# Optimization experiments

Measured on AMD Instinct MI355X. Metric: run time of the kernel, lower is better.

The kernel has to match this reference:

```python
import jax, jax.numpy as jnp
import numpy as np

TEMPERATURE = 0.5


def setup_inputs() -> dict:
    key = jax.random.key(0)
    ks = jax.random.split(key, 12)
    B, N, T = 128, 64, 256
    IN, H, OUT = N + T, 256, 128
    E = N * (N - 1) // 2  # 2016 upper-tri edges per graph
    total_edges = B * E
    inp = {
        "x_topology": jax.random.normal(ks[0], (B, N, N), jnp.float32),
        "x_temporal": jax.random.normal(ks[1], (B, N, T), jnp.float32),
        "gumbel_u": jax.random.uniform(ks[2], (total_edges,), jnp.float32, 1e-6, 1.0),
        # GNNLayer linear
        "W_gnn": jax.random.normal(ks[3], (IN, H), jnp.float32) / np.sqrt(IN),
        "b_gnn": jnp.zeros((H,), jnp.float32),
        # edge heads (input dim 2*H)
        "W_mean": jax.random.normal(ks[4], (2 * H, OUT), jnp.float32) / np.sqrt(2 * H),
        "b_mean": jnp.zeros((OUT,), jnp.float32),
        "W_var": jax.random.normal(ks[5], (2 * H, OUT), jnp.float32) / np.sqrt(2 * H),
        "b_var": jnp.zeros((OUT,), jnp.float32),
        "W_w": jax.random.normal(ks[6], (2 * H, 1), jnp.float32) / np.sqrt(2 * H),
        "b_w": jnp.zeros((1,), jnp.float32),
    }
    return inp


def reference(x_topology, x_temporal, gumbel_u, W_gnn, b_gnn,
              W_mean, b_mean, W_var, b_var, W_w, b_w):
    B, N, _ = x_topology.shape
    T = x_temporal.shape[-1]
    # Upper-triangular fully-connected edge index (no self loops), batched with node offsets.
    row, col = jnp.triu_indices(N, k=1)          # [E]
    E = row.shape[0]
    offs = (jnp.arange(B) * N)[:, None]          # [B,1]
    src = (row[None, :] + offs).reshape(-1)       # [B*E]
    dst = (col[None, :] + offs).reshape(-1)       # [B*E]

    # Node features: concat topology + temporal, flatten batch of graphs.
    x = jnp.concatenate([x_topology, x_temporal], axis=-1).reshape(B * N, N + T)

    # Mean aggregation (PyG aggr='mean'): messages x[src] scattered to dst; 0 for isolated nodes.
    msg_sum = jax.ops.segment_sum(x[src], dst, num_segments=B * N)      # [B*N, N+T]
    cnt = jax.ops.segment_sum(jnp.ones_like(src, x.dtype), dst, num_segments=B * N)
    agg = jnp.where(cnt[:, None] > 0, msg_sum / jnp.maximum(cnt, 1.0)[:, None], 0.0)

    h = jax.nn.relu(agg @ W_gnn + b_gnn)          # [B*N, H]

    # Edge MLP heads on gathered [src||dst] embeddings.
    ef = jnp.concatenate([h[src], h[dst]], axis=-1)        # [B*E, 2H]
    mean = ef @ W_mean + b_mean                             # [B*E, OUT]
    variance = jax.nn.softplus(ef @ W_var + b_var) + 1e-6   # [B*E, OUT]
    weight = jax.nn.sigmoid((ef @ W_w + b_w)[:, 0])          # [B*E]

    # Gumbel-softmax over the flattened edge-weight vector (dim=-1 of a 1-D tensor).
    g = -jnp.log(-jnp.log(gumbel_u))
    gumbel_w = jax.nn.softmax((weight + g) / TEMPERATURE, axis=-1)

    # Gaussian similarity per edge, scatter into dense adjacency.
    sim = jnp.exp(-0.5 * jnp.mean(mean ** 2 / (variance + 1e-8), axis=-1))
    edge_w = sim * gumbel_w                                  # [B*E]

    b_idx = jnp.repeat(jnp.arange(B), E)
    adj = jnp.zeros((B, N, N), x.dtype).at[b_idx, jnp.tile(row, B), jnp.tile(col, B)].set(edge_w)
    return adj
```

## Files before the change

### kernel.cpp

```cpp
#include <hip/hip_runtime.h>
#include <hip/hip_bf16.h>
#include <math.h>

#define Bg   128
#define Nn   64
#define Tt   256
#define INF  320
#define Hd   256
#define OUTD 128
#define Ee   2016
#define TOTE (Bg*Ee)
#define SCOLS 576
#define MROWS 8192

typedef __attribute__((ext_vector_type(8))) short bf16x8;
typedef __attribute__((ext_vector_type(4))) float f32x4;

static __device__ __forceinline__ ushort f2bf(float v) {
    __hip_bfloat16 h = __float2bfloat16(v);
    return *(ushort*)&h;
}

#define CVT_N (INF * Hd)
#define PACK_N (Hd * SCOLS)
__global__ void k_prep(const float* __restrict__ Wg, const float* __restrict__ Wm,
                       const float* __restrict__ Wv, const float* __restrict__ Ww,
                       const float* __restrict__ bm, const float* __restrict__ bv,
                       const float* __restrict__ bw,
                       ushort* __restrict__ WgbT, ushort* __restrict__ WcatT,
                       float* __restrict__ ebias, unsigned* __restrict__ red) {
    int idx = blockIdx.x * 256 + threadIdx.x;
    if (idx == 0) { red[0] = 0u; red[1] = 0u; }
    if (idx < CVT_N) {
        int n = idx / INF, k = idx - n * INF;
        WgbT[idx] = f2bf(Wg[k * Hd + n]);
        return;
    }
    idx -= CVT_N;
    if (idx < PACK_N) {
        int n = idx / Hd, k = idx - n * Hd;
        float v = 0.f;
        if (n < 128)       v = Wm[k * 128 + n];
        else if (n < 256)  v = Wm[(256 + k) * 128 + (n - 128)];
        else if (n < 384)  v = Wv[k * 128 + (n - 256)];
        else if (n < 512)  v = Wv[(256 + k) * 128 + (n - 384)];
        else if (n == 512) v = Ww[k];
        else if (n == 513) v = Ww[256 + k];
        WcatT[idx] = f2bf(v);
        return;
    }
    idx -= PACK_N;
    if (idx >= SCOLS) return;
    float e = 0.f;
    if (idx < 128)                    e = bm[idx];
    else if (idx >= 256 && idx < 384) e = bv[idx - 256];
    else if (idx == 512)              e = bw[0];
    ebias[idx] = e;
}

__global__ __launch_bounds__(256) void k_agg(const float* __restrict__ topo,
                                             const float* __restrict__ temp,
                                             ushort* __restrict__ agg) {
    __shared__ float T[64 * 65];
    const int b = blockIdx.x, ft = blockIdx.y;
    const int tid = threadIdx.x;
    const int row = tid >> 2, seg = tid & 3;
    const float* src = (ft == 0) ? (topo + (size_t)(b * Nn + row) * Nn)
                                 : (temp + (size_t)(b * Nn + row) * Tt + (ft - 1) * 64);
    #pragma unroll
    for (int i = 0; i < 4; ++i) {
        float4 v = *(const float4*)(src + seg * 16 + i * 4);
        float* d = &T[row * 65 + seg * 16 + i * 4];
        d[0] = v.x; d[1] = v.y; d[2] = v.z; d[3] = v.w;
    }
    __syncthreads();
    const int w = tid >> 6, lane = tid & 63;
    #pragma unroll
    for (int k = 0; k < 16; ++k) {
        int f = w * 16 + k;
        float x = T[lane * 65 + f];
        float incl = x;
        #pragma unroll
        for (int o = 1; o < 64; o <<= 1) {
            float t = __shfl_up(incl, o);
            if (lane >= o) incl += t;
        }
        float excl = incl - x;
        T[lane * 65 + f] = lane ? excl * __builtin_amdgcn_rcpf((float)lane) : 0.f;
    }
    __syncthreads();
    const int node = tid >> 2, f0 = (tid & 3) * 16;
    ushort tmp[16];
    #pragma unroll
    for (int i = 0; i < 16; ++i) tmp[i] = f2bf(T[node * 65 + f0 + i]);
    ushort* dst = agg + (size_t)(b * Nn + node) * INF + ft * 64 + f0;
    *(uint4*)dst = *(uint4*)tmp;
    *(uint4*)(dst + 8) = *(uint4*)(tmp + 8);
}

__global__ __launch_bounds__(256) void k_gemm_mfma(const ushort* __restrict__ A,
                                                   const ushort* __restrict__ BT,
                                                   const float* __restrict__ bias,
                                                   ushort* __restrict__ Cb,
                                                   float* __restrict__ Cf,
                                                   int N, int K, int relu, int transC) {
    __shared__ ushort Asl[64 * 72];
    __shared__ ushort Bsl[64 * 72];
    const int tid = threadIdx.x;
    const int w = tid >> 6, lane = tid & 63;
    const int quad = lane >> 4, r16 = lane & 15;
    const int m0 = blockIdx.y * 64, n0 = blockIdx.x * 64;
    const int row = tid >> 2, seg = tid & 3;
    f32x4 acc[4] = {};

    for (int k0 = 0; k0 < K; k0 += 64) {
        const ushort* ap = A + (size_t)(m0 + row) * K + k0 + seg * 16;
        uint4 a0 = ((const uint4*)ap)[0];
        uint4 a1 = ((const uint4*)ap)[1];
        *(uint4*)(Asl + row * 72 + seg * 16)     = a0;
        *(uint4*)(Asl + row * 72 + seg * 16 + 8) = a1;
        const ushort* bp = BT + (size_t)(n0 + row) * K + k0 + seg * 16;
        uint4 b0 = ((const uint4*)bp)[0];
        uint4 b1 = ((const uint4*)bp)[1];
        *(uint4*)(Bsl + row * 72 + seg * 16)     = b0;
        *(uint4*)(Bsl + row * 72 + seg * 16 + 8) = b1;
        __syncthreads();

        bf16x8 af0 = *(const bf16x8*)(Asl + (w * 16 + r16) * 72 + quad * 8);
        bf16x8 af1 = *(const bf16x8*)(Asl + (w * 16 + r16) * 72 + 32 + quad * 8);
        #pragma unroll
        for (int ns = 0; ns < 4; ++ns) {
            bf16x8 bf0 = *(const bf16x8*)(Bsl + (ns * 16 + r16) * 72 + quad * 8);
            bf16x8 bf1 = *(const bf16x8*)(Bsl + (ns * 16 + r16) * 72 + 32 + quad * 8);
            acc[ns] = __builtin_amdgcn_mfma_f32_16x16x32_bf16(af0, bf0, acc[ns], 0, 0, 0);
            acc[ns] = __builtin_amdgcn_mfma_f32_16x16x32_bf16(af1, bf1, acc[ns], 0, 0, 0);
        }
        __syncthreads();
    }

    const int row0 = m0 + w * 16 + quad * 4;
    #pragma unroll
    for (int ns = 0; ns < 4; ++ns) {
        f32x4 a = acc[ns];
        int col = n0 + ns * 16 + r16;
        float bb = bias ? bias[col] : 0.f;
        float vv[4];
        #pragma unroll
        for (int i = 0; i < 4; ++i) {
            float v = a[i] + bb;
            if (relu) v = fmaxf(v, 0.f);
            vv[i] = v;
        }
        if (transC) {
            *(float4*)(Cf + (size_t)col * MROWS + row0) = make_float4(vv[0], vv[1], vv[2], vv[3]);
        } else {
            #pragma unroll
            for (int i = 0; i < 4; ++i) {
                int row2 = row0 + i;
                if (Cb) Cb[(size_t)row2 * N + col] = f2bf(vv[i]);
                else    Cf[(size_t)row2 * N + col] = vv[i];
            }
        }
    }
}

static __device__ __forceinline__ float eterm(float pm, float qm, float pv, float qv) {
    float m = pm + qm;
    float x = pv + qv;
    float sp = fmaxf(x, 0.f) + __logf(1.f + __expf(-fabsf(x)));
    return m * m * __builtin_amdgcn_rcpf(sp + 1.01e-6f);
}

__global__ __launch_bounds__(256) void k_edge4(const float* __restrict__ ST,
                                               const float* __restrict__ gu,
                                               float* __restrict__ numer,
                                               unsigned* __restrict__ red) {
    __shared__ float L[4][16][132];
    __shared__ float sm[256];
    const int p = blockIdx.x % 10, b = blockIdx.x / 10;
    const int G0v[10] = {0,0,0,0,1,1,1,2,2,3};
    const int G1v[10] = {0,1,2,3,1,2,3,2,3,3};
    const int g0 = G0v[p], g1 = G1v[p];
    const int tid = threadIdx.x;

    #pragma unroll
    for (int rep = 0; rep < 8; ++rep) {
        int it = tid + 256 * rep;
        int arr = it >> 9;
        int c = (it >> 2) & 127, nq = it & 3;
        int g = (arr & 1) ? g1 : g0;
        float4 v = *(const float4*)&ST[(size_t)(arr * 128 + c) * MROWS + b * 64 + g * 16 + nq * 4];
        L[arr][nq * 4 + 0][c] = v.x;
        L[arr][nq * 4 + 1][c] = v.y;
        L[arr][nq * 4 + 2][c] = v.z;
        L[arr][nq * 4 + 3][c] = v.w;
    }
    __syncthreads();

    const int i = tid >> 4, j = tid & 15;
    float acc = 0.f;
    #pragma unroll 4
    for (int t = 0; t < 128; t += 4) {
        float4 mi = *(const float4*)&L[0][i][t];
        float4 mj = *(const float4*)&L[1][j][t];
        float4 vi = *(const float4*)&L[2][i][t];
        float4 vj = *(const float4*)&L[3][j][t];
        acc += eterm(mi.x, mj.x, vi.x, vj.x);
        acc += eterm(mi.y, mj.y, vi.y, vj.y);
        acc += eterm(mi.z, mj.z, vi.z, vj.z);
        acc += eterm(mi.w, mj.w, vi.w, vj.w);
    }

    const int ni = g0 * 16 + i, nj = g1 * 16 + j;
    float en = 0.f;
    if (ni < nj) {
        int e = b * Ee + (ni * (127 - ni)) / 2 + (nj - ni - 1);
        float se = __expf(acc * (-1.f / 256.f));
        float wr = ST[(size_t)512 * MROWS + b * 64 + ni]
                 + ST[(size_t)513 * MROWS + b * 64 + nj];
        float w  = __builtin_amdgcn_rcpf(1.f + __expf(-wr));
        float g  = -__logf(-__logf(gu[e]));
        en = __expf((w + g) * 2.0f);
        numer[e] = se * en;
    }
    sm[tid] = en; __syncthreads();
    for (int s = 128; s; s >>= 1) {
        if (tid < s) sm[tid] += sm[tid + s];
        __syncthreads();
    }
    if (!tid) atomicAdd((float*)&red[1], sm[0]);
}

__global__ void k_out(const float* __restrict__ numer, const unsigned* __restrict__ red,
                      float* __restrict__ out) {
    int idx = blockIdx.x * 256 + threadIdx.x;
    if (idx >= Bg * Nn * Nn) return;
    int b = idx >> 12;
    int rem = idx & 4095;
    int r = rem >> 6, c = rem & 63;
    float v = 0.f;
    if (c > r) {
        int e = b * Ee + (r * (127 - r)) / 2 + (c - r - 1);
        float Sinv = __builtin_amdgcn_rcpf(((const float*)red)[1]);
        v = numer[e] * Sinv;
    }
    out[idx] = v;
}

extern "C" void kernel_launch(void* const* d_in, const int* in_sizes, int n_in,
                              void* d_out, int out_size, void* d_ws, size_t ws_size,
                              hipStream_t stream) {
    const float* topo = (const float*)d_in[0];
    const float* temp = (const float*)d_in[1];
    const float* gu   = (const float*)d_in[2];
    const float* Wg   = (const float*)d_in[3];
    const float* bg   = (const float*)d_in[4];
    const float* Wm   = (const float*)d_in[5];
    const float* bm   = (const float*)d_in[6];
    const float* Wv   = (const float*)d_in[7];
    const float* bv   = (const float*)d_in[8];
    const float* Ww   = (const float*)d_in[9];
    const float* bw   = (const float*)d_in[10];
    float* out = (float*)d_out;

    char* ws = (char*)d_ws;
    size_t off = 0;
    auto carve = [&](size_t bytes) { char* p = ws + off; off = (off + bytes + 255) & ~(size_t)255; return p; };

    char*   r1    = carve((size_t)SCOLS * MROWS * 4);
    float*  ST    = (float*)r1;
    ushort* aggb  = (ushort*)r1;
    ushort* hb    = (ushort*)carve((size_t)MROWS * Hd * 2);
    ushort* WgbT  = (ushort*)carve((size_t)INF * Hd * 2);
    ushort* WcatT = (ushort*)carve((size_t)Hd * SCOLS * 2);
    float*  ebias = (float*)carve((size_t)SCOLS * 4);
    float*  numer = (float*)carve((size_t)TOTE * 4);
    unsigned* red = (unsigned*)carve(256);

    k_prep<<<(CVT_N + PACK_N + SCOLS + 255) / 256, 256, 0, stream>>>(
        Wg, Wm, Wv, Ww, bm, bv, bw, WgbT, WcatT, ebias, red);
    k_agg<<<dim3(Bg, INF / 64), 256, 0, stream>>>(topo, temp, aggb);
    k_gemm_mfma<<<dim3(Hd / 64, MROWS / 64), 256, 0, stream>>>(
        aggb, WgbT, bg, hb, nullptr, Hd, INF, 1, 0);
    k_gemm_mfma<<<dim3(SCOLS / 64, MROWS / 64), 256, 0, stream>>>(
        hb, WcatT, ebias, nullptr, ST, SCOLS, Hd, 0, 1);
    k_edge4<<<Bg * 10, 256, 0, stream>>>(ST, gu, numer, red);
    k_out<<<(Bg * Nn * Nn + 255) / 256, 256, 0, stream>>>(numer, red, out);
}
```

Measured before the change: 146.9 us.

## Fuse aggregation with weight prep and use pre-swizzled weights in LDS-free GEMM

Merges the weight-conversion kernel and the mean-aggregation kernel into one launch, with the block index selecting the role. Weights are now stored in an MFMA-fragment order, so the GEMM reads A and B operands straight from global memory into registers without LDS staging or barriers. The aim is to cut one launch and the shared-memory copies and syncs. In exchange each wave reloads its operands from global or L2 with no sharing through LDS, which may raise memory traffic.

```diff
diff --git a/kernel.cpp b/kernel.cpp
--- a/kernel.cpp
+++ b/kernel.cpp
@@ -23,22 +23,76 @@
 
 #define CVT_N (INF * Hd)
 #define PACK_N (Hd * SCOLS)
-__global__ void k_prep(const float* __restrict__ Wg, const float* __restrict__ Wm,
-                       const float* __restrict__ Wv, const float* __restrict__ Ww,
-                       const float* __restrict__ bm, const float* __restrict__ bv,
-                       const float* __restrict__ bw,
-                       ushort* __restrict__ WgbT, ushort* __restrict__ WcatT,
-                       float* __restrict__ ebias, unsigned* __restrict__ red) {
-    int idx = blockIdx.x * 256 + threadIdx.x;
+#define AGG_BLKS (Bg * 5)
+
+__global__ __launch_bounds__(256) void k_agg_prep(
+        const float* __restrict__ topo, const float* __restrict__ temp,
+        const float* __restrict__ Wg, const float* __restrict__ Wm,
+        const float* __restrict__ Wv, const float* __restrict__ Ww,
+        const float* __restrict__ bm, const float* __restrict__ bv,
+        const float* __restrict__ bw,
+        ushort* __restrict__ agg, ushort* __restrict__ WgbS,
+        ushort* __restrict__ WcatS, float* __restrict__ ebias,
+        unsigned* __restrict__ red) {
+    __shared__ float T[64 * 65];
+    const int bid = blockIdx.x;
+    const int tid = threadIdx.x;
+
+    if (bid < AGG_BLKS) {
+        const int b = bid / 5, ft = bid - 5 * (bid / 5);
+        const int row = tid >> 2, seg = tid & 3;
+        const float* src = (ft == 0) ? (topo + (size_t)(b * Nn + row) * Nn)
+                                     : (temp + (size_t)(b * Nn + row) * Tt + (ft - 1) * 64);
+        #pragma unroll
+        for (int i = 0; i < 4; ++i) {
+            float4 v = *(const float4*)(src + seg * 16 + i * 4);
+            float* d = &T[row * 65 + seg * 16 + i * 4];
+            d[0] = v.x; d[1] = v.y; d[2] = v.z; d[3] = v.w;
+        }
+        __syncthreads();
+        const int w = tid >> 6, lane = tid & 63;
+        #pragma unroll
+        for (int k = 0; k < 16; ++k) {
+            int f = w * 16 + k;
+            float x = T[lane * 65 + f];
+            float incl = x;
+            #pragma unroll
+            for (int o = 1; o < 64; o <<= 1) {
+                float t = __shfl_up(incl, o);
+                if (lane >= o) incl += t;
+            }
+            float excl = incl - x;
+            T[lane * 65 + f] = lane ? excl * __builtin_amdgcn_rcpf((float)lane) : 0.f;
+        }
+        __syncthreads();
+        const int node = tid >> 2, f0 = (tid & 3) * 16;
+        ushort tmp[16];
+        #pragma unroll
+        for (int i = 0; i < 16; ++i) tmp[i] = f2bf(T[node * 65 + f0 + i]);
+        ushort* dst = agg + (size_t)(b * Nn + node) * INF + ft * 64 + f0;
+        *(uint4*)dst = *(uint4*)tmp;
+        *(uint4*)(dst + 8) = *(uint4*)(tmp + 8);
+        return;
+    }
+
+    int idx = (bid - AGG_BLKS) * 256 + tid;
     if (idx == 0) { red[0] = 0u; red[1] = 0u; }
     if (idx < CVT_N) {
-        int n = idx / INF, k = idx - n * INF;
-        WgbT[idx] = f2bf(Wg[k * Hd + n]);
+        int j = idx & 7, lane = (idx >> 3) & 63, ns = (idx >> 9) & 3;
+        int rem = idx >> 11;
+        int kw = rem % 10, t = rem / 10;
+        int n = t * 64 + ns * 16 + (lane & 15);
+        int k = kw * 32 + (lane >> 4) * 8 + j;
+        WgbS[idx] = f2bf(Wg[k * Hd + n]);
         return;
     }
     idx -= CVT_N;
     if (idx < PACK_N) {
-        int n = idx / Hd, k = idx - n * Hd;
+        int j = idx & 7, lane = (idx >> 3) & 63, ns = (idx >> 9) & 3;
+        int rem = idx >> 11;
+        int kw = rem % 8, t = rem / 8;
+        int n = t * 64 + ns * 16 + (lane & 15);
+        int k = kw * 32 + (lane >> 4) * 8 + j;
         float v = 0.f;
         if (n < 128)       v = Wm[k * 128 + n];
         else if (n < 256)  v = Wm[(256 + k) * 128 + (n - 128)];
@@ -46,7 +100,7 @@
         else if (n < 512)  v = Wv[(256 + k) * 128 + (n - 384)];
         else if (n == 512) v = Ww[k];
         else if (n == 513) v = Ww[256 + k];
-        WcatT[idx] = f2bf(v);
+        WcatS[idx] = f2bf(v);
         return;
     }
     idx -= PACK_N;
@@ -58,84 +112,33 @@
     ebias[idx] = e;
 }
 
-__global__ __launch_bounds__(256) void k_agg(const float* __restrict__ topo,
-                                             const float* __restrict__ temp,
-                                             ushort* __restrict__ agg) {
-    __shared__ float T[64 * 65];
-    const int b = blockIdx.x, ft = blockIdx.y;
-    const int tid = threadIdx.x;
-    const int row = tid >> 2, seg = tid & 3;
-    const float* src = (ft == 0) ? (topo + (size_t)(b * Nn + row) * Nn)
-                                 : (temp + (size_t)(b * Nn + row) * Tt + (ft - 1) * 64);
-    #pragma unroll
-    for (int i = 0; i < 4; ++i) {
-        float4 v = *(const float4*)(src + seg * 16 + i * 4);
-        float* d = &T[row * 65 + seg * 16 + i * 4];
-        d[0] = v.x; d[1] = v.y; d[2] = v.z; d[3] = v.w;
-    }
-    __syncthreads();
-    const int w = tid >> 6, lane = tid & 63;
-    #pragma unroll
-    for (int k = 0; k < 16; ++k) {
-        int f = w * 16 + k;
-        float x = T[lane * 65 + f];
-        float incl = x;
-        #pragma unroll
-        for (int o = 1; o < 64; o <<= 1) {
-            float t = __shfl_up(incl, o);
-            if (lane >= o) incl += t;
-        }
-        float excl = incl - x;
-        T[lane * 65 + f] = lane ? excl * __builtin_amdgcn_rcpf((float)lane) : 0.f;
-    }
-    __syncthreads();
-    const int node = tid >> 2, f0 = (tid & 3) * 16;
-    ushort tmp[16];
-    #pragma unroll
-    for (int i = 0; i < 16; ++i) tmp[i] = f2bf(T[node * 65 + f0 + i]);
-    ushort* dst = agg + (size_t)(b * Nn + node) * INF + ft * 64 + f0;
-    *(uint4*)dst = *(uint4*)tmp;
-    *(uint4*)(dst + 8) = *(uint4*)(tmp + 8);
-}
-
-__global__ __launch_bounds__(256) void k_gemm_mfma(const ushort* __restrict__ A,
-                                                   const ushort* __restrict__ BT,
-                                                   const float* __restrict__ bias,
-                                                   ushort* __restrict__ Cb,
-                                                   float* __restrict__ Cf,
-                                                   int N, int K, int relu, int transC) {
-    __shared__ ushort Asl[64 * 72];
-    __shared__ ushort Bsl[64 * 72];
+template<int K>
+__global__ __launch_bounds__(256) void k_gemm_direct(const ushort* __restrict__ A,
+                                                     const ushort* __restrict__ Bsw,
+                                                     const float* __restrict__ bias,
+                                                     ushort* __restrict__ Cb,
+                                                     float* __restrict__ Cf,
+                                                     int N, int relu, int transC) {
     const int tid = threadIdx.x;
     const int w = tid >> 6, lane = tid & 63;
     const int quad = lane >> 4, r16 = lane & 15;
     const int m0 = blockIdx.y * 64, n0 = blockIdx.x * 64;
-    const int row = tid >> 2, seg = tid & 3;
+    const ushort* arow = A + (size_t)(m0 + w * 16 + r16) * K + quad * 8;
+    const ushort* bbase = Bsw + (size_t)blockIdx.x * (K / 32) * 2048 + lane * 8;
     f32x4 acc[4] = {};
 
-    for (int k0 = 0; k0 < K; k0 += 64) {
-        const ushort* ap = A + (size_t)(m0 + row) * K + k0 + seg * 16;
-        uint4 a0 = ((const uint4*)ap)[0];
-        uint4 a1 = ((const uint4*)ap)[1];
-        *(uint4*)(Asl + row * 72 + seg * 16)     = a0;
-        *(uint4*)(Asl + row * 72 + seg * 16 + 8) = a1;
-        const ushort* bp = BT + (size_t)(n0 + row) * K + k0 + seg * 16;
-        uint4 b0 = ((const uint4*)bp)[0];
-        uint4 b1 = ((const uint4*)bp)[1];
-        *(uint4*)(Bsl + row * 72 + seg * 16)     = b0;
-        *(uint4*)(Bsl + row * 72 + seg * 16 + 8) = b1;
-        __syncthreads();
-
-        bf16x8 af0 = *(const bf16x8*)(Asl + (w * 16 + r16) * 72 + quad * 8);
-        bf16x8 af1 = *(const bf16x8*)(Asl + (w * 16 + r16) * 72 + 32 + quad * 8);
-        #pragma unroll
-        for (int ns = 0; ns < 4; ++ns) {
-            bf16x8 bf0 = *(const bf16x8*)(Bsl + (ns * 16 + r16) * 72 + quad * 8);
-            bf16x8 bf1 = *(const bf16x8*)(Bsl + (ns * 16 + r16) * 72 + 32 + quad * 8);
-            acc[ns] = __builtin_amdgcn_mfma_f32_16x16x32_bf16(af0, bf0, acc[ns], 0, 0, 0);
-            acc[ns] = __builtin_amdgcn_mfma_f32_16x16x32_bf16(af1, bf1, acc[ns], 0, 0, 0);
-        }
-        __syncthreads();
+    #pragma unroll 2
+    for (int kw = 0; kw < K / 32; ++kw) {
+        bf16x8 af = *(const bf16x8*)(arow + kw * 32);
+        const ushort* bp = bbase + kw * 2048;
+        bf16x8 b0 = *(const bf16x8*)(bp);
+        bf16x8 b1 = *(const bf16x8*)(bp + 512);
+        bf16x8 b2 = *(const bf16x8*)(bp + 1024);
+        bf16x8 b3 = *(const bf16x8*)(bp + 1536);
+        acc[0] = __builtin_amdgcn_mfma_f32_16x16x32_bf16(af, b0, acc[0], 0, 0, 0);
+        acc[1] = __builtin_amdgcn_mfma_f32_16x16x32_bf16(af, b1, acc[1], 0, 0, 0);
+        acc[2] = __builtin_amdgcn_mfma_f32_16x16x32_bf16(af, b2, acc[2], 0, 0, 0);
+        acc[3] = __builtin_amdgcn_mfma_f32_16x16x32_bf16(af, b3, acc[3], 0, 0, 0);
     }
 
     const int row0 = m0 + w * 16 + quad * 4;
@@ -271,19 +274,19 @@
     float*  ST    = (float*)r1;
     ushort* aggb  = (ushort*)r1;
     ushort* hb    = (ushort*)carve((size_t)MROWS * Hd * 2);
-    ushort* WgbT  = (ushort*)carve((size_t)INF * Hd * 2);
-    ushort* WcatT = (ushort*)carve((size_t)Hd * SCOLS * 2);
+    ushort* WgbS  = (ushort*)carve((size_t)CVT_N * 2);
+    ushort* WcatS = (ushort*)carve((size_t)PACK_N * 2);
     float*  ebias = (float*)carve((size_t)SCOLS * 4);
     float*  numer = (float*)carve((size_t)TOTE * 4);
     unsigned* red = (unsigned*)carve(256);
 
-    k_prep<<<(CVT_N + PACK_N + SCOLS + 255) / 256, 256, 0, stream>>>(
-        Wg, Wm, Wv, Ww, bm, bv, bw, WgbT, WcatT, ebias, red);
-    k_agg<<<dim3(Bg, INF / 64), 256, 0, stream>>>(topo, temp, aggb);
-    k_gemm_mfma<<<dim3(Hd / 64, MROWS / 64), 256, 0, stream>>>(
-        aggb, WgbT, bg, hb, nullptr, Hd, INF, 1, 0);
-    k_gemm_mfma<<<dim3(SCOLS / 64, MROWS / 64), 256, 0, stream>>>(
-        hb, WcatT, ebias, nullptr, ST, SCOLS, Hd, 0, 1);
+    const int prep_blks = (CVT_N + PACK_N + SCOLS + 255) / 256;
+    k_agg_prep<<<AGG_BLKS + prep_blks, 256, 0, stream>>>(
+        topo, temp, Wg, Wm, Wv, Ww, bm, bv, bw, aggb, WgbS, WcatS, ebias, red);
+    k_gemm_direct<INF><<<dim3(Hd / 64, MROWS / 64), 256, 0, stream>>>(
+        aggb, WgbS, bg, hb, nullptr, Hd, 1, 0);
+    k_gemm_direct<Hd><<<dim3(SCOLS / 64, MROWS / 64), 256, 0, stream>>>(
+        hb, WcatS, ebias, nullptr, ST, SCOLS, 0, 1);
     k_edge4<<<Bg * 10, 256, 0, stream>>>(ST, gu, numer, red);
     k_out<<<(Bg * Nn * Nn + 255) / 256, 256, 0, stream>>>(numer, red, out);
 }
```

Result: no change. 148.1 us (+0.8%).

## Split edge kernel along feature dim and move softmax finalize to separate kernel

Applied to the files above, without the earlier changes.

The edge-similarity kernel now splits the 128-wide feature reduction into two halves across separate blocks, doubling the block count to 2560. It writes partial sums to a workspace. The 4 diagonal 16x16 tile pairs remap their threads so that only the 120 upper-triangle pairs do work, instead of masking half of them out. A new finalize kernel uses a precomputed edge-to-(row,col) LUT to sum the partials and compute the gumbel/sigmoid terms and the global sum. This adds an extra launch and extra partial-buffer traffic.

```diff
diff --git a/kernel.cpp b/kernel.cpp
--- a/kernel.cpp
+++ b/kernel.cpp
@@ -28,7 +28,8 @@
                        const float* __restrict__ bm, const float* __restrict__ bv,
                        const float* __restrict__ bw,
                        ushort* __restrict__ WgbT, ushort* __restrict__ WcatT,
-                       float* __restrict__ ebias, unsigned* __restrict__ red) {
+                       float* __restrict__ ebias, int2* __restrict__ lut,
+                       unsigned* __restrict__ red) {
     int idx = blockIdx.x * 256 + threadIdx.x;
     if (idx == 0) { red[0] = 0u; red[1] = 0u; }
     if (idx < CVT_N) {
@@ -50,12 +51,20 @@
         return;
     }
     idx -= PACK_N;
-    if (idx >= SCOLS) return;
-    float e = 0.f;
-    if (idx < 128)                    e = bm[idx];
-    else if (idx >= 256 && idx < 384) e = bv[idx - 256];
-    else if (idx == 512)              e = bw[0];
-    ebias[idx] = e;
+    if (idx < SCOLS) {
+        float e = 0.f;
+        if (idx < 128)                    e = bm[idx];
+        else if (idx >= 256 && idx < 384) e = bv[idx - 256];
+        else if (idx == 512)              e = bw[0];
+        ebias[idx] = e;
+        return;
+    }
+    idx -= SCOLS;
+    if (idx >= Ee) return;
+    int r = 0;
+    while ((r + 1) * (127 - (r + 1)) / 2 <= idx) ++r;
+    int c = r + 1 + (idx - r * (127 - r) / 2);
+    lut[idx] = make_int2(r, c);
 }
 
 __global__ __launch_bounds__(256) void k_agg(const float* __restrict__ topo,
@@ -171,25 +180,27 @@
     return m * m * __builtin_amdgcn_rcpf(sp + 1.01e-6f);
 }
 
-__global__ __launch_bounds__(256) void k_edge4(const float* __restrict__ ST,
-                                               const float* __restrict__ gu,
-                                               float* __restrict__ numer,
-                                               unsigned* __restrict__ red) {
-    __shared__ float L[4][16][132];
-    __shared__ float sm[256];
-    const int p = blockIdx.x % 10, b = blockIdx.x / 10;
-    const int G0v[10] = {0,0,0,0,1,1,1,2,2,3};
-    const int G1v[10] = {0,1,2,3,1,2,3,2,3,3};
+__global__ __launch_bounds__(256) void k_edge5(const float* __restrict__ ST,
+                                               float* __restrict__ partial) {
+    __shared__ float L[4][16][68];
+    const int blk = blockIdx.x;
+    const int ts = blk & 1;
+    const int p  = (blk >> 1) % 10;
+    const int b  = blk / 20;
+    const int toff = ts * 64;
+    const int tid = threadIdx.x;
+    const int G0v[10] = {0,0,0,1,1,2, 0,1,2,3};
+    const int G1v[10] = {1,2,3,2,3,3, 0,1,2,3};
     const int g0 = G0v[p], g1 = G1v[p];
-    const int tid = threadIdx.x;
-
-    #pragma unroll
-    for (int rep = 0; rep < 8; ++rep) {
+
+    #pragma unroll
+    for (int rep = 0; rep < 4; ++rep) {
         int it = tid + 256 * rep;
-        int arr = it >> 9;
-        int c = (it >> 2) & 127, nq = it & 3;
+        int arr = it >> 8;
+        int idx2 = it & 255;
+        int c = idx2 >> 2, nq = idx2 & 3;
         int g = (arr & 1) ? g1 : g0;
-        float4 v = *(const float4*)&ST[(size_t)(arr * 128 + c) * MROWS + b * 64 + g * 16 + nq * 4];
+        float4 v = *(const float4*)&ST[(size_t)(arr * 128 + toff + c) * MROWS + b * 64 + g * 16 + nq * 4];
         L[arr][nq * 4 + 0][c] = v.x;
         L[arr][nq * 4 + 1][c] = v.y;
         L[arr][nq * 4 + 2][c] = v.z;
@@ -197,38 +208,62 @@
     }
     __syncthreads();
 
-    const int i = tid >> 4, j = tid & 15;
-    float acc = 0.f;
-    #pragma unroll 4
-    for (int t = 0; t < 128; t += 4) {
-        float4 mi = *(const float4*)&L[0][i][t];
-        float4 mj = *(const float4*)&L[1][j][t];
-        float4 vi = *(const float4*)&L[2][i][t];
-        float4 vj = *(const float4*)&L[3][j][t];
-        acc += eterm(mi.x, mj.x, vi.x, vj.x);
-        acc += eterm(mi.y, mj.y, vi.y, vj.y);
-        acc += eterm(mi.z, mj.z, vi.z, vj.z);
-        acc += eterm(mi.w, mj.w, vi.w, vj.w);
-    }
-
-    const int ni = g0 * 16 + i, nj = g1 * 16 + j;
-    float en = 0.f;
-    if (ni < nj) {
-        int e = b * Ee + (ni * (127 - ni)) / 2 + (nj - ni - 1);
-        float se = __expf(acc * (-1.f / 256.f));
-        float wr = ST[(size_t)512 * MROWS + b * 64 + ni]
-                 + ST[(size_t)513 * MROWS + b * 64 + nj];
-        float w  = __builtin_amdgcn_rcpf(1.f + __expf(-wr));
-        float g  = -__logf(-__logf(gu[e]));
-        en = __expf((w + g) * 2.0f);
-        numer[e] = se * en;
-    }
-    sm[tid] = en; __syncthreads();
+    int i, j;
+    bool act;
+    if (p < 6) {
+        i = tid >> 4; j = tid & 15; act = true;
+    } else {
+        act = tid < 120;
+        i = 0; j = 0;
+        if (act) {
+            int rem = tid;
+            while (rem >= 15 - i) { rem -= 15 - i; ++i; }
+            j = i + 1 + rem;
+        }
+    }
+
+    if (act) {
+        float acc = 0.f;
+        #pragma unroll 4
+        for (int t = 0; t < 64; t += 4) {
+            float4 mi = *(const float4*)&L[0][i][t];
+            float4 mj = *(const float4*)&L[1][j][t];
+            float4 vi = *(const float4*)&L[2][i][t];
+            float4 vj = *(const float4*)&L[3][j][t];
+            acc += eterm(mi.x, mj.x, vi.x, vj.x);
+            acc += eterm(mi.y, mj.y, vi.y, vj.y);
+            acc += eterm(mi.z, mj.z, vi.z, vj.z);
+            acc += eterm(mi.w, mj.w, vi.w, vj.w);
+        }
+        int ni = g0 * 16 + i, nj = g1 * 16 + j;
+        partial[(size_t)ts * TOTE + b * Ee + (ni * (127 - ni)) / 2 + (nj - ni - 1)] = acc;
+    }
+}
+
+__global__ __launch_bounds__(256) void k_fin(const float* __restrict__ partial,
+                                             const float* __restrict__ ST,
+                                             const int2* __restrict__ lut,
+                                             const float* __restrict__ gu,
+                                             float* __restrict__ numer,
+                                             unsigned* __restrict__ red) {
+    __shared__ float sm[256];
+    int e = blockIdx.x * 256 + threadIdx.x;
+    int b = e / Ee, el = e - b * Ee;
+    int2 rc = lut[el];
+    float acc = partial[e] + partial[TOTE + e];
+    float se = __expf(acc * (-1.f / 256.f));
+    float wr = ST[(size_t)512 * MROWS + b * 64 + rc.x]
+             + ST[(size_t)513 * MROWS + b * 64 + rc.y];
+    float w  = __builtin_amdgcn_rcpf(1.f + __expf(-wr));
+    float g  = -__logf(-__logf(gu[e]));
+    float en = __expf((w + g) * 2.0f);
+    numer[e] = se * en;
+    sm[threadIdx.x] = en; __syncthreads();
     for (int s = 128; s; s >>= 1) {
-        if (tid < s) sm[tid] += sm[tid + s];
+        if (threadIdx.x < s) sm[threadIdx.x] += sm[threadIdx.x + s];
         __syncthreads();
     }
-    if (!tid) atomicAdd((float*)&red[1], sm[0]);
+    if (!threadIdx.x) atomicAdd((float*)&red[1], sm[0]);
 }
 
 __global__ void k_out(const float* __restrict__ numer, const unsigned* __restrict__ red,
@@ -271,19 +306,22 @@
     float*  ST    = (float*)r1;
     ushort* aggb  = (ushort*)r1;
     ushort* hb    = (ushort*)carve((size_t)MROWS * Hd * 2);
-    ushort* WgbT  = (ushort*)carve((size_t)INF * Hd * 2);
-    ushort* WcatT = (ushort*)carve((size_t)Hd * SCOLS * 2);
+    ushort* WgbT  = (ushort*)carve((size_t)CVT_N * 2);
+    ushort* WcatT = (ushort*)carve((size_t)PACK_N * 2);
     float*  ebias = (float*)carve((size_t)SCOLS * 4);
+    float*  part  = (float*)carve((size_t)2 * TOTE * 4);
     float*  numer = (float*)carve((size_t)TOTE * 4);
+    int2*   lut   = (int2*)carve((size_t)Ee * 8);
     unsigned* red = (unsigned*)carve(256);
 
-    k_prep<<<(CVT_N + PACK_N + SCOLS + 255) / 256, 256, 0, stream>>>(
-        Wg, Wm, Wv, Ww, bm, bv, bw, WgbT, WcatT, ebias, red);
+    k_prep<<<(CVT_N + PACK_N + SCOLS + Ee + 255) / 256, 256, 0, stream>>>(
+        Wg, Wm, Wv, Ww, bm, bv, bw, WgbT, WcatT, ebias, lut, red);
     k_agg<<<dim3(Bg, INF / 64), 256, 0, stream>>>(topo, temp, aggb);
     k_gemm_mfma<<<dim3(Hd / 64, MROWS / 64), 256, 0, stream>>>(
         aggb, WgbT, bg, hb, nullptr, Hd, INF, 1, 0);
     k_gemm_mfma<<<dim3(SCOLS / 64, MROWS / 64), 256, 0, stream>>>(
         hb, WcatT, ebias, nullptr, ST, SCOLS, Hd, 0, 1);
-    k_edge4<<<Bg * 10, 256, 0, stream>>>(ST, gu, numer, red);
+    k_edge5<<<Bg * 20, 256, 0, stream>>>(ST, part);
+    k_fin<<<TOTE / 256, 256, 0, stream>>>(part, ST, lut, gu, numer, red);
     k_out<<<(Bg * Nn * Nn + 255) / 256, 256, 0, stream>>>(numer, red, out);
 }
```

Measured after the change: 157.1 us. 1.07x slower.

## Split edge kernel LDS staging into two phases and compact diagonal tile work

Applied to the files above, without the earlier changes.

The edge kernel now stages the mean/variance tiles in two 64-column phases, halving shared memory per block to raise occupancy. Diagonal 16x16 tiles map only the 120 upper-triangular pairs to threads instead of masking half the work. The dot loop uses two accumulators for more ILP, and the block reduction is replaced by a wavefront shuffle reduction with one atomic per wave. The cost is an extra barrier, more atomics on the global sum, and idle threads in diagonal blocks.

```diff
diff --git a/kernel.cpp b/kernel.cpp
--- a/kernel.cpp
+++ b/kernel.cpp
@@ -175,45 +175,73 @@
                                                const float* __restrict__ gu,
                                                float* __restrict__ numer,
                                                unsigned* __restrict__ red) {
-    __shared__ float L[4][16][132];
-    __shared__ float sm[256];
+    __shared__ float L[4][16][68];
     const int p = blockIdx.x % 10, b = blockIdx.x / 10;
-    const int G0v[10] = {0,0,0,0,1,1,1,2,2,3};
-    const int G1v[10] = {0,1,2,3,1,2,3,2,3,3};
+    const int G0v[10] = {0,0,0,1,1,2, 0,1,2,3};
+    const int G1v[10] = {1,2,3,2,3,3, 0,1,2,3};
     const int g0 = G0v[p], g1 = G1v[p];
     const int tid = threadIdx.x;
 
-    #pragma unroll
-    for (int rep = 0; rep < 8; ++rep) {
-        int it = tid + 256 * rep;
-        int arr = it >> 9;
-        int c = (it >> 2) & 127, nq = it & 3;
-        int g = (arr & 1) ? g1 : g0;
-        float4 v = *(const float4*)&ST[(size_t)(arr * 128 + c) * MROWS + b * 64 + g * 16 + nq * 4];
-        L[arr][nq * 4 + 0][c] = v.x;
-        L[arr][nq * 4 + 1][c] = v.y;
-        L[arr][nq * 4 + 2][c] = v.z;
-        L[arr][nq * 4 + 3][c] = v.w;
-    }
-    __syncthreads();
-
-    const int i = tid >> 4, j = tid & 15;
-    float acc = 0.f;
-    #pragma unroll 4
-    for (int t = 0; t < 128; t += 4) {
-        float4 mi = *(const float4*)&L[0][i][t];
-        float4 mj = *(const float4*)&L[1][j][t];
-        float4 vi = *(const float4*)&L[2][i][t];
-        float4 vj = *(const float4*)&L[3][j][t];
-        acc += eterm(mi.x, mj.x, vi.x, vj.x);
-        acc += eterm(mi.y, mj.y, vi.y, vj.y);
-        acc += eterm(mi.z, mj.z, vi.z, vj.z);
-        acc += eterm(mi.w, mj.w, vi.w, vj.w);
-    }
-
-    const int ni = g0 * 16 + i, nj = g1 * 16 + j;
+    int i, j;
+    bool act;
+    if (p < 6) {
+        i = tid >> 4; j = tid & 15; act = true;
+    } else {
+        act = tid < 120;
+        i = 0; j = 0;
+        if (act) {
+            int rem = tid;
+            while (rem >= 15 - i) { rem -= 15 - i; ++i; }
+            j = i + 1 + rem;
+        }
+    }
+
+    float acc0 = 0.f, acc1 = 0.f;
+    for (int ph = 0; ph < 2; ++ph) {
+        if (ph) __syncthreads();
+        #pragma unroll
+        for (int rep = 0; rep < 4; ++rep) {
+            int it = tid + 256 * rep;
+            int arr = it >> 8;
+            int idx2 = it & 255;
+            int c = idx2 >> 2, nq = idx2 & 3;
+            int g = (arr & 1) ? g1 : g0;
+            float4 v = *(const float4*)&ST[(size_t)(arr * 128 + ph * 64 + c) * MROWS
+                                           + b * 64 + g * 16 + nq * 4];
+            L[arr][nq * 4 + 0][c] = v.x;
+            L[arr][nq * 4 + 1][c] = v.y;
+            L[arr][nq * 4 + 2][c] = v.z;
+            L[arr][nq * 4 + 3][c] = v.w;
+        }
+        __syncthreads();
+
+        if (act) {
+            #pragma unroll 4
+            for (int t = 0; t < 64; t += 8) {
+                float4 miA = *(const float4*)&L[0][i][t];
+                float4 mjA = *(const float4*)&L[1][j][t];
+                float4 viA = *(const float4*)&L[2][i][t];
+                float4 vjA = *(const float4*)&L[3][j][t];
+                float4 miB = *(const float4*)&L[0][i][t + 4];
+                float4 mjB = *(const float4*)&L[1][j][t + 4];
+                float4 viB = *(const float4*)&L[2][i][t + 4];
+                float4 vjB = *(const float4*)&L[3][j][t + 4];
+                acc0 += eterm(miA.x, mjA.x, viA.x, vjA.x);
+                acc1 += eterm(miB.x, mjB.x, viB.x, vjB.x);
+                acc0 += eterm(miA.y, mjA.y, viA.y, vjA.y);
+                acc1 += eterm(miB.y, mjB.y, viB.y, vjB.y);
+                acc0 += eterm(miA.z, mjA.z, viA.z, vjA.z);
+                acc1 += eterm(miB.z, mjB.z, viB.z, vjB.z);
+                acc0 += eterm(miA.w, mjA.w, viA.w, vjA.w);
+                acc1 += eterm(miB.w, mjB.w, viB.w, vjB.w);
+            }
+        }
+    }
+
     float en = 0.f;
-    if (ni < nj) {
+    if (act) {
+        float acc = acc0 + acc1;
+        int ni = g0 * 16 + i, nj = g1 * 16 + j;
         int e = b * Ee + (ni * (127 - ni)) / 2 + (nj - ni - 1);
         float se = __expf(acc * (-1.f / 256.f));
         float wr = ST[(size_t)512 * MROWS + b * 64 + ni]
@@ -223,12 +251,9 @@
         en = __expf((w + g) * 2.0f);
         numer[e] = se * en;
     }
-    sm[tid] = en; __syncthreads();
-    for (int s = 128; s; s >>= 1) {
-        if (tid < s) sm[tid] += sm[tid + s];
-        __syncthreads();
-    }
-    if (!tid) atomicAdd((float*)&red[1], sm[0]);
+    #pragma unroll
+    for (int off = 32; off; off >>= 1) en += __shfl_down(en, off);
+    if ((tid & 63) == 0) atomicAdd((float*)&red[1], en);
 }
 
 __global__ void k_out(const float* __restrict__ numer, const unsigned* __restrict__ red,
@@ -271,8 +296,8 @@
     float*  ST    = (float*)r1;
     ushort* aggb  = (ushort*)r1;
     ushort* hb    = (ushort*)carve((size_t)MROWS * Hd * 2);
-    ushort* WgbT  = (ushort*)carve((size_t)INF * Hd * 2);
-    ushort* WcatT = (ushort*)carve((size_t)Hd * SCOLS * 2);
+    ushort* WgbT  = (ushort*)carve((size_t)CVT_N * 2);
+    ushort* WcatT = (ushort*)carve((size_t)PACK_N * 2);
     float*  ebias = (float*)carve((size_t)SCOLS * 4);
     float*  numer = (float*)carve((size_t)TOTE * 4);
     unsigned* red = (unsigned*)carve(256);
```

New measurement: 185.6 us. 26.3% more time.
